# Performance work log

Hardware: AMD Instinct MI355X
Metric: run time of the kernel (lower is better)

## Reference

```python
import jax, jax.numpy as jnp
import numpy as np

N_RAYS = 8192
N_SAMPLES = 128
HIDDEN = 128
SH_DIM = 16
RAY_EXT_FACTOR = 10.0


def rsh_cart_3(d):
    # Real spherical harmonics up to degree 3, Cartesian form (16 coeffs).
    x, y, z = d[..., 0], d[..., 1], d[..., 2]
    x2, y2, z2 = x * x, y * y, z * z
    xy, yz, xz = x * y, y * z, x * z
    return jnp.stack([
        0.282094791773878 * jnp.ones_like(x),
        -0.48860251190292 * y,
        0.48860251190292 * z,
        -0.48860251190292 * x,
        1.0925484305920792 * xy,
        -1.0925484305920792 * yz,
        0.94617469575756 * z2 - 0.31539156525252,
        -1.0925484305920792 * xz,
        0.5462742152960396 * (x2 - y2),
        0.5900435899266435 * y * (-3.0 * x2 + y2),
        2.8906114426405538 * xy * z,
        0.4570457994644658 * y * (1.0 - 5.0 * z2),
        0.3731763325901154 * z * (5.0 * z2 - 3.0),
        0.4570457994644658 * x * (1.0 - 5.0 * z2),
        1.445305721320277 * z * (x2 - y2),
        0.5900435899266435 * x * (-x2 + 3.0 * y2),
    ], axis=-1)


def setup_inputs() -> dict:
    key = jax.random.key(0)
    ks = jax.random.split(key, 11)
    o = jax.random.normal(ks[0], (N_RAYS, 3), dtype=jnp.float32)
    origins = 2.5 * o / jnp.linalg.norm(o, axis=-1, keepdims=True)
    # aim roughly at the unit AABB so most rays are active
    dirs = -origins + 0.2 * jax.random.normal(ks[1], (N_RAYS, 3), dtype=jnp.float32)
    u = jax.random.uniform(ks[2], (N_RAYS, N_SAMPLES), dtype=jnp.float32)
    s1 = 1.0 / np.sqrt(3.0)
    s2 = 1.0 / np.sqrt(HIDDEN)
    s3 = 1.0 / np.sqrt(HIDDEN + SH_DIM)
    return {
        'origins': origins,
        'dirs': dirs,
        'u': u,
        'W1': s1 * jax.random.normal(ks[3], (3, HIDDEN), dtype=jnp.float32),
        'b1': jnp.zeros((HIDDEN,), jnp.float32),
        'W2': s2 * jax.random.normal(ks[4], (HIDDEN, HIDDEN), dtype=jnp.float32),
        'b2': jnp.zeros((HIDDEN,), jnp.float32),
        'Wd': s2 * jax.random.normal(ks[5], (HIDDEN, 1), dtype=jnp.float32),
        'bd': jnp.zeros((1,), jnp.float32),
        'Wc': s3 * jax.random.normal(ks[6], (HIDDEN + SH_DIM, 3), dtype=jnp.float32),
        'bc': jnp.zeros((3,), jnp.float32),
    }


def reference(origins, dirs, u, W1, b1, W2, b2, Wd, bd, Wc, bc):
    B, T = u.shape
    # ---- AABB ([-1,1]^3) slab intersection -> tnear/tfar, active mask ----
    inv_d = 1.0 / dirs
    t1 = (-1.0 - origins) * inv_d
    t2 = (1.0 - origins) * inv_d
    tnear = jnp.maximum(jnp.max(jnp.minimum(t1, t2), axis=-1), 0.0)  # (B,)
    tfar = jnp.min(jnp.maximum(t1, t2), axis=-1)                      # (B,)
    active = tfar > tnear                                             # (B,)
    tfar_c = jnp.maximum(tfar, tnear + 1e-3)
    # ---- stratified ray step sampling ----
    frac = (jnp.arange(T, dtype=u.dtype) + u) / T                     # (B,T)
    ts = tnear[:, None] + (tfar_c - tnear)[:, None] * frac            # (B,T)
    xyz = origins[:, None, :] + dirs[:, None, :] * ts[..., None]      # (B,T,3)
    # aabb is [-1,1]^3 so ndc == xyz; spatial filter = bounds test
    xyz_ndc = xyz
    mask = jnp.all(jnp.abs(xyz_ndc) <= 1.0, axis=-1) & active[:, None]  # (B,T)
    dnorm = jnp.linalg.norm(dirs, axis=-1)                            # (B,)
    ynm = rsh_cart_3(dirs / dnorm[:, None])                           # (B,16)
    # ---- radiance field MLP over all sample points ----
    x = xyz_ndc.reshape(B * T, 3)
    h = jax.nn.relu(x @ W1 + b1)
    h = jax.nn.relu(h @ W2 + b2)
    sigma = jax.nn.softplus(h @ Wd + bd).reshape(B, T)
    cond = jnp.broadcast_to(ynm[:, None, :], (B, T, SH_DIM)).reshape(B * T, SH_DIM)
    color = jax.nn.sigmoid(jnp.concatenate([h, cond], axis=-1) @ Wc + bc).reshape(B, T, 3)
    # zero out points rejected by the spatial filter (torch writes only masked)
    sigma = sigma * mask
    color = color * mask[..., None]
    # ---- transmittance integration (integrate_timesteps) ----
    tfinal = tfar_c * RAY_EXT_FACTOR
    deltas = jnp.diff(ts, axis=-1, append=tfinal[:, None])            # (B,T)
    sd = sigma * deltas * dnorm[:, None]
    csum = jnp.cumsum(sd, axis=-1)
    # weights_i = T_i * alpha_i = exp(-csum_{i-1}) - exp(-csum_i)
    weights = jnp.exp(sd - csum) - jnp.exp(-csum)                     # (B,T)
    color_out = jnp.einsum('bt,btc->bc', weights, color)              # (B,3)
    alpha_out = jnp.sum(weights, axis=-1, keepdims=True)              # (B,1)
    rgba = jnp.concatenate([color_out, alpha_out], axis=-1)           # (B,4)
    return jnp.where(active[:, None], rgba, 0.0)
```

## Files before the change

### kernel.cpp

```cpp
#include <hip/hip_runtime.h>
#include <math.h>

#define NRAYS 8192
#define T 128
#define H 128
#define SHD 16

using short8 = __attribute__((ext_vector_type(8))) short;
using f32x4  = __attribute__((ext_vector_type(4))) float;
using f32x2  = __attribute__((ext_vector_type(2))) float;
using u32x2  = __attribute__((ext_vector_type(2))) unsigned;

__device__ __forceinline__ float fexp(float x) {
  return exp2f(x * 1.44269504088896341f);
}
__device__ __forceinline__ float softplus_f(float x) {
  return fmaxf(x, 0.f) + 0.693147180559945309f * log2f(1.f + fexp(-fabsf(x)));
}
__device__ __forceinline__ float sigmoid_f(float x) {
  return __builtin_amdgcn_rcpf(1.f + fexp(-x));
}

__device__ __forceinline__ unsigned f2bf(float f) {
  unsigned u = __float_as_uint(f);
  return (u + 0x7fffu + ((u >> 16) & 1u)) >> 16;
}

__device__ __forceinline__ unsigned pk2(f32x2 h) {
  const u32x2 u = __builtin_bit_cast(u32x2, h) + (u32x2){0x8000u, 0x8000u};
  return __builtin_amdgcn_perm(u[1], u[0], 0x07060302u);
}

__global__ void preprocess(const float* __restrict__ W2, const float* __restrict__ Wd,
                           const float* __restrict__ Wc, const float* __restrict__ bc,
                           const float* __restrict__ origins, const float* __restrict__ dirs,
                           unsigned short* __restrict__ w2t,
                           unsigned short* __restrict__ woutf,
                           float* __restrict__ rayp_all) {
  const int t = blockIdx.x * 256 + threadIdx.x;
  if (t < 16384) {
    const int n = t >> 7, p = t & 127;
    const int o = (p >> 3) ^ (n & 7);
    const int k = o * 8 + (p & 7);
    w2t[t] = (unsigned short)f2bf(W2[k * 128 + n]);
  }
  if (t < 2048) {
    const int kk = t >> 9, L = (t >> 3) & 63, j = t & 7;
    const int c = L & 15, g = L >> 4;
    const int k = kk * 32 + g * 8 + j;
    float v = 0.f;
    if (c == 0) v = Wd[k];
    else if (c < 4) v = Wc[k * 3 + (c - 1)];
    woutf[t] = (unsigned short)f2bf(v);
  }
  if (t < NRAYS) {
    const float ox = origins[t*3+0], oy = origins[t*3+1], oz = origins[t*3+2];
    const float dx = dirs[t*3+0],  dy = dirs[t*3+1],  dz = dirs[t*3+2];
    const float ix = 1.f/dx, iy = 1.f/dy, iz = 1.f/dz;
    const float t1x = (-1.f-ox)*ix, t2x = (1.f-ox)*ix;
    const float t1y = (-1.f-oy)*iy, t2y = (1.f-oy)*iy;
    const float t1z = (-1.f-oz)*iz, t2z = (1.f-oz)*iz;
    float tnear = fmaxf(fmaxf(fminf(t1x,t2x), fminf(t1y,t2y)), fminf(t1z,t2z));
    tnear = fmaxf(tnear, 0.f);
    const float tfar = fminf(fminf(fmaxf(t1x,t2x), fmaxf(t1y,t2y)), fmaxf(t1z,t2z));
    const bool  active = tfar > tnear;
    const float tfar_c = fmaxf(tfar, tnear + 1e-3f);
    const float dnorm = sqrtf(dx*dx + dy*dy + dz*dz);
    const float nx = dx/dnorm, ny = dy/dnorm, nz = dz/dnorm;
    const float x2 = nx*nx, y2 = ny*ny, z2 = nz*nz;
    const float xy = nx*ny, yz = ny*nz, xz = nx*nz;
    float ynm[16];
    ynm[0]  = 0.282094791773878f;
    ynm[1]  = -0.48860251190292f*ny;
    ynm[2]  = 0.48860251190292f*nz;
    ynm[3]  = -0.48860251190292f*nx;
    ynm[4]  = 1.0925484305920792f*xy;
    ynm[5]  = -1.0925484305920792f*yz;
    ynm[6]  = 0.94617469575756f*z2 - 0.31539156525252f;
    ynm[7]  = -1.0925484305920792f*xz;
    ynm[8]  = 0.5462742152960396f*(x2-y2);
    ynm[9]  = 0.5900435899266435f*ny*(-3.f*x2+y2);
    ynm[10] = 2.8906114426405538f*xy*nz;
    ynm[11] = 0.4570457994644658f*ny*(1.f-5.f*z2);
    ynm[12] = 0.3731763325901154f*nz*(5.f*z2-3.f);
    ynm[13] = 0.4570457994644658f*nx*(1.f-5.f*z2);
    ynm[14] = 1.445305721320277f*nz*(x2-y2);
    ynm[15] = 0.5900435899266435f*nx*(-x2+3.f*y2);
    float cp0 = bc[0], cp1 = bc[1], cp2 = bc[2];
    #pragma unroll
    for (int s = 0; s < SHD; ++s) {
      cp0 = fmaf(ynm[s], Wc[(H+s)*3+0], cp0);
      cp1 = fmaf(ynm[s], Wc[(H+s)*3+1], cp1);
      cp2 = fmaf(ynm[s], Wc[(H+s)*3+2], cp2);
    }
    rayp_all[t*8+0] = tfar_c;
    rayp_all[t*8+1] = dnorm;
    rayp_all[t*8+2] = active ? 1.f : 0.f;
    rayp_all[t*8+3] = cp0;
    rayp_all[t*8+4] = cp1;
    rayp_all[t*8+5] = cp2;
    rayp_all[t*8+6] = tnear;
    rayp_all[t*8+7] = 0.f;
  }
}

__global__ __launch_bounds__(256, 4) void nerf_render(
    const float* __restrict__ origins, const float* __restrict__ dirs,
    const float* __restrict__ u, const float* __restrict__ W1,
    const float* __restrict__ b1, const float* __restrict__ b2,
    const float* __restrict__ bd, const unsigned short* __restrict__ w2t,
    const unsigned short* __restrict__ woutf, const float* __restrict__ rayp_all,
    float* __restrict__ out)
{
  const int ray = blockIdx.x;
  const int tid = threadIdx.x;
  const int L = tid & 63;
  const int w = tid >> 6;
  const int g = L >> 4;
  const int c = L & 15;

  __shared__ __align__(16) short Bs[16384];
  __shared__ __align__(16) short As2[4 * 640];
  __shared__ __align__(16) float baseA[H];
  __shared__ __align__(16) float slopeA[H];
  __shared__ float ts_s[T];
  __shared__ float mask_s[T];
  __shared__ float wred[2][4];
  __shared__ float wtot[2];

  const float tfar_c = rayp_all[ray*8+0];
  const float dnorm  = rayp_all[ray*8+1];
  const float actf   = rayp_all[ray*8+2];
  const float cpo0   = rayp_all[ray*8+3];
  const float cpo1   = rayp_all[ray*8+4];
  const float cpo2   = rayp_all[ray*8+5];
  const float tnear  = rayp_all[ray*8+6];

  {
    const float4* src = (const float4*)w2t;
    float4* dst = (float4*)Bs;
    #pragma unroll
    for (int i = 0; i < 8; ++i) dst[tid + i * 256] = src[tid + i * 256];
  }

  if (tid < T) {
    const int tl = tid;
    const float ox = origins[ray*3+0], oy = origins[ray*3+1], oz = origins[ray*3+2];
    const float dx = dirs[ray*3+0],  dy = dirs[ray*3+1],  dz = dirs[ray*3+2];
    const bool active = actf != 0.f;
    const float ut = u[ray*T + tl];
    const float frac = ((float)tl + ut) * (1.f/(float)T);
    const float tt = tnear + (tfar_c - tnear) * frac;
    const float px = fmaf(dx, tt, ox);
    const float py = fmaf(dy, tt, oy);
    const float pz = fmaf(dz, tt, oz);
    ts_s[tl] = tt;
    const bool m = (fabsf(px) <= 1.f) && (fabsf(py) <= 1.f) && (fabsf(pz) <= 1.f) && active;
    mask_s[tl] = m ? 1.f : 0.f;
    const float w0 = W1[tl], w1v = W1[H + tl], w2v = W1[2*H + tl];
    baseA[tl]  = fmaf(ox, w0, fmaf(oy, w1v, fmaf(oz, w2v, b1[tl])));
    slopeA[tl] = fmaf(dx, w0, fmaf(dy, w1v, dz * w2v));
  }

  f32x4 acc[2][8];
  #pragma unroll
  for (int mt = 0; mt < 8; ++mt) {
    const float4 bv = *(const float4*)&b2[mt*16 + g*4];
    #pragma unroll
    for (int tm = 0; tm < 2; ++tm) {
      acc[tm][mt][0] = bv.x; acc[tm][mt][1] = bv.y;
      acc[tm][mt][2] = bv.z; acc[tm][mt][3] = bv.w;
    }
  }
  __syncthreads();

  const float t0 = ts_s[32*w + c];
  const float t1 = ts_s[32*w + 16 + c];
  const f32x2 tz0 = {t0, t0}, tz1 = {t1, t1};
  const f32x2 zero2 = {0.f, 0.f};

  #pragma unroll
  for (int ks = 0; ks < 4; ++ks) {
    const int kb = ks*32 + g*8;
    const f32x4 bq0 = *(const f32x4*)&baseA[kb];
    const f32x4 bq1 = *(const f32x4*)&baseA[kb+4];
    const f32x4 sq0 = *(const f32x4*)&slopeA[kb];
    const f32x4 sq1 = *(const f32x4*)&slopeA[kb+4];
    const f32x2 b01 = {bq0[0], bq0[1]}, b23 = {bq0[2], bq0[3]};
    const f32x2 b45 = {bq1[0], bq1[1]}, b67 = {bq1[2], bq1[3]};
    const f32x2 s01 = {sq0[0], sq0[1]}, s23 = {sq0[2], sq0[3]};
    const f32x2 s45 = {sq1[0], sq1[1]}, s67 = {sq1[2], sq1[3]};
    const f32x2 a01 = __builtin_elementwise_max(__builtin_elementwise_fma(tz0, s01, b01), zero2);
    const f32x2 a23 = __builtin_elementwise_max(__builtin_elementwise_fma(tz0, s23, b23), zero2);
    const f32x2 a45 = __builtin_elementwise_max(__builtin_elementwise_fma(tz0, s45, b45), zero2);
    const f32x2 a67 = __builtin_elementwise_max(__builtin_elementwise_fma(tz0, s67, b67), zero2);
    const f32x2 e01 = __builtin_elementwise_max(__builtin_elementwise_fma(tz1, s01, b01), zero2);
    const f32x2 e23 = __builtin_elementwise_max(__builtin_elementwise_fma(tz1, s23, b23), zero2);
    const f32x2 e45 = __builtin_elementwise_max(__builtin_elementwise_fma(tz1, s45, b45), zero2);
    const f32x2 e67 = __builtin_elementwise_max(__builtin_elementwise_fma(tz1, s67, b67), zero2);
    union U { uint4 u; short8 s; } A0, A1;
    A0.u = make_uint4(pk2(a01), pk2(a23), pk2(a45), pk2(a67));
    A1.u = make_uint4(pk2(e01), pk2(e23), pk2(e45), pk2(e67));
    const int swb = ((ks*4 + g) ^ (c & 7)) * 8;
    #pragma unroll
    for (int mt = 0; mt < 8; ++mt) {
      const short8 wf = *(const short8*)&Bs[(mt*16 + c)*128 + swb];
      acc[0][mt] = __builtin_amdgcn_mfma_f32_16x16x32_bf16(wf, A0.s, acc[0][mt], 0, 0, 0);
      acc[1][mt] = __builtin_amdgcn_mfma_f32_16x16x32_bf16(wf, A1.s, acc[1][mt], 0, 0, 0);
    }
  }
  __syncthreads();
  float4* SredP = (float4*)Bs;

  short* As2w = As2 + w * 640;
  short8 wa[4];
  #pragma unroll
  for (int kk = 0; kk < 4; ++kk)
    wa[kk] = *(const short8*)&woutf[(kk*64 + L)*8];

  #pragma unroll
  for (int tm = 0; tm < 2; ++tm) {
    f32x4 oacc;
    oacc[0] = 0.f; oacc[1] = 0.f; oacc[2] = 0.f; oacc[3] = 0.f;
    #pragma unroll
    for (int kk = 0; kk < 4; ++kk) {
      #pragma unroll
      for (int i = 0; i < 2; ++i) {
        const f32x4 a = acc[tm][kk*2 + i];
        const f32x2 h01 = __builtin_elementwise_max((f32x2){a[0], a[1]}, zero2);
        const f32x2 h23 = __builtin_elementwise_max((f32x2){a[2], a[3]}, zero2);
        *(uint2*)&As2w[c*40 + i*16 + g*4] = make_uint2(pk2(h01), pk2(h23));
      }
      const short8 hbf = *(const short8*)&As2w[c*40 + g*8];
      oacc = __builtin_amdgcn_mfma_f32_16x16x32_bf16(wa[kk], hbf, oacc, 0, 0, 0);
    }
    if (g == 0)
      SredP[32*w + 16*tm + c] = make_float4(oacc[0], oacc[1], oacc[2], oacc[3]);
  }
  __syncthreads();

  float sd = 0.f, cc0 = 0.f, cc1 = 0.f, cc2 = 0.f;
  if (tid < T) {
    const float4 sv = SredP[tid];
    const float mk = mask_s[tid];
    const float sigma = softplus_f(sv.x + bd[0]) * mk;
    cc0 = mk * sigmoid_f(sv.y + cpo0);
    cc1 = mk * sigmoid_f(sv.z + cpo1);
    cc2 = mk * sigmoid_f(sv.w + cpo2);
    const float tt = ts_s[tid];
    const float tnext = (tid < T-1) ? ts_s[tid + 1] : tfar_c * 10.f;
    sd = sigma * (tnext - tt) * dnorm;
  }

  float val = sd;
  #pragma unroll
  for (int off = 1; off < 64; off <<= 1) {
    const float tmp = __shfl_up(val, off);
    if (L >= off) val += tmp;
  }
  if (tid < T && L == 63) wtot[w] = val;
  __syncthreads();
  const float csum = val + ((w == 1) ? wtot[0] : 0.f);

  float wgt = 0.f, wcx = 0.f, wcy = 0.f, wcz = 0.f;
  if (tid < T) {
    wgt = fexp(sd - csum) - fexp(-csum);
    wcx = wgt * cc0; wcy = wgt * cc1; wcz = wgt * cc2;
  }
  #pragma unroll
  for (int mm = 32; mm >= 1; mm >>= 1) {
    wgt += __shfl_xor(wgt, mm);
    wcx += __shfl_xor(wcx, mm);
    wcy += __shfl_xor(wcy, mm);
    wcz += __shfl_xor(wcz, mm);
  }
  if (tid < T && L == 0) {
    wred[w][0] = wgt; wred[w][1] = wcx; wred[w][2] = wcy; wred[w][3] = wcz;
  }
  __syncthreads();
  if (tid == 0) {
    const float aw = wred[0][0] + wred[1][0];
    const float o0 = wred[0][1] + wred[1][1];
    const float o1 = wred[0][2] + wred[1][2];
    const float o2 = wred[0][3] + wred[1][3];
    const bool act = actf != 0.f;
    out[ray*4+0] = act ? o0 : 0.f;
    out[ray*4+1] = act ? o1 : 0.f;
    out[ray*4+2] = act ? o2 : 0.f;
    out[ray*4+3] = act ? aw : 0.f;
  }
}

extern "C" void kernel_launch(void* const* d_in, const int* in_sizes, int n_in,
                              void* d_out, int out_size, void* d_ws, size_t ws_size,
                              hipStream_t stream) {
  const float* origins = (const float*)d_in[0];
  const float* dirs    = (const float*)d_in[1];
  const float* u       = (const float*)d_in[2];
  const float* W1      = (const float*)d_in[3];
  const float* b1      = (const float*)d_in[4];
  const float* W2      = (const float*)d_in[5];
  const float* b2      = (const float*)d_in[6];
  const float* Wd      = (const float*)d_in[7];
  const float* bd      = (const float*)d_in[8];
  const float* Wc      = (const float*)d_in[9];
  const float* bc      = (const float*)d_in[10];

  unsigned short* w2t      = (unsigned short*)d_ws;
  unsigned short* woutf    = (unsigned short*)((char*)d_ws + 32768);
  float*          rayp_all = (float*)((char*)d_ws + 36864);

  preprocess<<<64, 256, 0, stream>>>(W2, Wd, Wc, bc, origins, dirs,
                                     w2t, woutf, rayp_all);
  nerf_render<<<NRAYS, 256, 0, stream>>>(origins, dirs, u, W1, b1, b2, bd,
                                         w2t, woutf, rayp_all, (float*)d_out);
}
```

Measured before the change: 132.1 us.

## Retile hidden GEMM as 2x2 wave grid and use DPP wave scans

The 128x128 hidden-layer MFMA is re-partitioned so each wave covers 64 output neurons by 64 samples (4x4 tiles) rather than all 128 neurons by 32 samples. This halves the LDS weight-fragment loads per MFMA, and each wave now builds only four activation fragments per k-step instead of two per eight weight loads. Because the output head is split across neuron halves, partial density and color sums are written to two LDS slots and added before the activations. The shuffle-based prefix scan and reductions are replaced with DPP row/bcast scans plus readlane, which cuts cross-lane latency at the cost of more bespoke lane-control code.

```diff
diff --git a/kernel.cpp b/kernel.cpp
--- a/kernel.cpp
+++ b/kernel.cpp
@@ -29,6 +29,25 @@
 __device__ __forceinline__ unsigned pk2(f32x2 h) {
   const u32x2 u = __builtin_bit_cast(u32x2, h) + (u32x2){0x8000u, 0x8000u};
   return __builtin_amdgcn_perm(u[1], u[0], 0x07060302u);
+}
+
+template<int CTRL, int RM>
+__device__ __forceinline__ float dppadd(float v) {
+  const int t = __builtin_amdgcn_update_dpp(0, __builtin_bit_cast(int, v), CTRL, RM, 0xf, false);
+  return v + __builtin_bit_cast(float, t);
+}
+__device__ __forceinline__ float wave_iscan(float v) {
+  v = dppadd<0x111, 0xf>(v);
+  v = dppadd<0x112, 0xf>(v);
+  v = dppadd<0x114, 0xf>(v);
+  v = dppadd<0x118, 0xf>(v);
+  v = dppadd<0x142, 0xa>(v);
+  v = dppadd<0x143, 0xc>(v);
+  return v;
+}
+__device__ __forceinline__ float wave_total(float v) {
+  v = wave_iscan(v);
+  return __builtin_bit_cast(float, __builtin_amdgcn_readlane(__builtin_bit_cast(int, v), 63));
 }
 
 __global__ void preprocess(const float* __restrict__ W2, const float* __restrict__ Wd,
@@ -116,6 +135,8 @@
   const int tid = threadIdx.x;
   const int L = tid & 63;
   const int w = tid >> 6;
+  const int wh = w >> 1;
+  const int ws = w & 1;
   const int g = L >> 4;
   const int c = L & 15;
 
@@ -162,21 +183,22 @@
     slopeA[tl] = fmaf(dx, w0, fmaf(dy, w1v, dz * w2v));
   }
 
-  f32x4 acc[2][8];
-  #pragma unroll
-  for (int mt = 0; mt < 8; ++mt) {
-    const float4 bv = *(const float4*)&b2[mt*16 + g*4];
-    #pragma unroll
-    for (int tm = 0; tm < 2; ++tm) {
-      acc[tm][mt][0] = bv.x; acc[tm][mt][1] = bv.y;
-      acc[tm][mt][2] = bv.z; acc[tm][mt][3] = bv.w;
+  f32x4 acc[4][4];
+  #pragma unroll
+  for (int mi = 0; mi < 4; ++mi) {
+    const float4 bv = *(const float4*)&b2[(wh*4 + mi)*16 + g*4];
+    #pragma unroll
+    for (int tn = 0; tn < 4; ++tn) {
+      acc[tn][mi][0] = bv.x; acc[tn][mi][1] = bv.y;
+      acc[tn][mi][2] = bv.z; acc[tn][mi][3] = bv.w;
     }
   }
   __syncthreads();
 
-  const float t0 = ts_s[32*w + c];
-  const float t1 = ts_s[32*w + 16 + c];
-  const f32x2 tz0 = {t0, t0}, tz1 = {t1, t1};
+  float t_tn[4];
+  #pragma unroll
+  for (int tn = 0; tn < 4; ++tn) t_tn[tn] = ts_s[64*ws + 16*tn + c];
+
   const f32x2 zero2 = {0.f, 0.f};
 
   #pragma unroll
@@ -190,74 +212,73 @@
     const f32x2 b45 = {bq1[0], bq1[1]}, b67 = {bq1[2], bq1[3]};
     const f32x2 s01 = {sq0[0], sq0[1]}, s23 = {sq0[2], sq0[3]};
     const f32x2 s45 = {sq1[0], sq1[1]}, s67 = {sq1[2], sq1[3]};
-    const f32x2 a01 = __builtin_elementwise_max(__builtin_elementwise_fma(tz0, s01, b01), zero2);
-    const f32x2 a23 = __builtin_elementwise_max(__builtin_elementwise_fma(tz0, s23, b23), zero2);
-    const f32x2 a45 = __builtin_elementwise_max(__builtin_elementwise_fma(tz0, s45, b45), zero2);
-    const f32x2 a67 = __builtin_elementwise_max(__builtin_elementwise_fma(tz0, s67, b67), zero2);
-    const f32x2 e01 = __builtin_elementwise_max(__builtin_elementwise_fma(tz1, s01, b01), zero2);
-    const f32x2 e23 = __builtin_elementwise_max(__builtin_elementwise_fma(tz1, s23, b23), zero2);
-    const f32x2 e45 = __builtin_elementwise_max(__builtin_elementwise_fma(tz1, s45, b45), zero2);
-    const f32x2 e67 = __builtin_elementwise_max(__builtin_elementwise_fma(tz1, s67, b67), zero2);
-    union U { uint4 u; short8 s; } A0, A1;
-    A0.u = make_uint4(pk2(a01), pk2(a23), pk2(a45), pk2(a67));
-    A1.u = make_uint4(pk2(e01), pk2(e23), pk2(e45), pk2(e67));
+
     const int swb = ((ks*4 + g) ^ (c & 7)) * 8;
-    #pragma unroll
-    for (int mt = 0; mt < 8; ++mt) {
-      const short8 wf = *(const short8*)&Bs[(mt*16 + c)*128 + swb];
-      acc[0][mt] = __builtin_amdgcn_mfma_f32_16x16x32_bf16(wf, A0.s, acc[0][mt], 0, 0, 0);
-      acc[1][mt] = __builtin_amdgcn_mfma_f32_16x16x32_bf16(wf, A1.s, acc[1][mt], 0, 0, 0);
+    short8 wf[4];
+    #pragma unroll
+    for (int mi = 0; mi < 4; ++mi)
+      wf[mi] = *(const short8*)&Bs[((wh*4 + mi)*16 + c)*128 + swb];
+
+    #pragma unroll
+    for (int tn = 0; tn < 4; ++tn) {
+      const f32x2 t2 = {t_tn[tn], t_tn[tn]};
+      const f32x2 a01 = __builtin_elementwise_max(__builtin_elementwise_fma(t2, s01, b01), zero2);
+      const f32x2 a23 = __builtin_elementwise_max(__builtin_elementwise_fma(t2, s23, b23), zero2);
+      const f32x2 a45 = __builtin_elementwise_max(__builtin_elementwise_fma(t2, s45, b45), zero2);
+      const f32x2 a67 = __builtin_elementwise_max(__builtin_elementwise_fma(t2, s67, b67), zero2);
+      union U { uint4 u; short8 s; } Bf;
+      Bf.u = make_uint4(pk2(a01), pk2(a23), pk2(a45), pk2(a67));
+      #pragma unroll
+      for (int mi = 0; mi < 4; ++mi)
+        acc[tn][mi] = __builtin_amdgcn_mfma_f32_16x16x32_bf16(wf[mi], Bf.s, acc[tn][mi], 0, 0, 0);
     }
   }
   __syncthreads();
-  float4* SredP = (float4*)Bs;
+  float4* SredH = (float4*)Bs;
 
   short* As2w = As2 + w * 640;
-  short8 wa[4];
-  #pragma unroll
-  for (int kk = 0; kk < 4; ++kk)
-    wa[kk] = *(const short8*)&woutf[(kk*64 + L)*8];
-
-  #pragma unroll
-  for (int tm = 0; tm < 2; ++tm) {
+  short8 wa2[2];
+  #pragma unroll
+  for (int i = 0; i < 2; ++i)
+    wa2[i] = *(const short8*)&woutf[((2*wh + i)*64 + L)*8];
+
+  #pragma unroll
+  for (int tn = 0; tn < 4; ++tn) {
     f32x4 oacc;
     oacc[0] = 0.f; oacc[1] = 0.f; oacc[2] = 0.f; oacc[3] = 0.f;
     #pragma unroll
-    for (int kk = 0; kk < 4; ++kk) {
+    for (int i = 0; i < 2; ++i) {
       #pragma unroll
-      for (int i = 0; i < 2; ++i) {
-        const f32x4 a = acc[tm][kk*2 + i];
+      for (int q = 0; q < 2; ++q) {
+        const int mi = 2*i + q;
+        const f32x4 a = acc[tn][mi];
         const f32x2 h01 = __builtin_elementwise_max((f32x2){a[0], a[1]}, zero2);
         const f32x2 h23 = __builtin_elementwise_max((f32x2){a[2], a[3]}, zero2);
-        *(uint2*)&As2w[c*40 + i*16 + g*4] = make_uint2(pk2(h01), pk2(h23));
+        *(uint2*)&As2w[c*40 + q*16 + g*4] = make_uint2(pk2(h01), pk2(h23));
       }
       const short8 hbf = *(const short8*)&As2w[c*40 + g*8];
-      oacc = __builtin_amdgcn_mfma_f32_16x16x32_bf16(wa[kk], hbf, oacc, 0, 0, 0);
+      oacc = __builtin_amdgcn_mfma_f32_16x16x32_bf16(wa2[i], hbf, oacc, 0, 0, 0);
     }
     if (g == 0)
-      SredP[32*w + 16*tm + c] = make_float4(oacc[0], oacc[1], oacc[2], oacc[3]);
+      SredH[wh*128 + 64*ws + 16*tn + c] = make_float4(oacc[0], oacc[1], oacc[2], oacc[3]);
   }
   __syncthreads();
 
   float sd = 0.f, cc0 = 0.f, cc1 = 0.f, cc2 = 0.f;
   if (tid < T) {
-    const float4 sv = SredP[tid];
+    const float4 sv0 = SredH[tid];
+    const float4 sv1 = SredH[128 + tid];
     const float mk = mask_s[tid];
-    const float sigma = softplus_f(sv.x + bd[0]) * mk;
-    cc0 = mk * sigmoid_f(sv.y + cpo0);
-    cc1 = mk * sigmoid_f(sv.z + cpo1);
-    cc2 = mk * sigmoid_f(sv.w + cpo2);
+    const float sigma = softplus_f(sv0.x + sv1.x + bd[0]) * mk;
+    cc0 = mk * sigmoid_f(sv0.y + sv1.y + cpo0);
+    cc1 = mk * sigmoid_f(sv0.z + sv1.z + cpo1);
+    cc2 = mk * sigmoid_f(sv0.w + sv1.w + cpo2);
     const float tt = ts_s[tid];
     const float tnext = (tid < T-1) ? ts_s[tid + 1] : tfar_c * 10.f;
     sd = sigma * (tnext - tt) * dnorm;
   }
 
-  float val = sd;
-  #pragma unroll
-  for (int off = 1; off < 64; off <<= 1) {
-    const float tmp = __shfl_up(val, off);
-    if (L >= off) val += tmp;
-  }
+  const float val = wave_iscan(sd);
   if (tid < T && L == 63) wtot[w] = val;
   __syncthreads();
   const float csum = val + ((w == 1) ? wtot[0] : 0.f);
@@ -267,15 +288,12 @@
     wgt = fexp(sd - csum) - fexp(-csum);
     wcx = wgt * cc0; wcy = wgt * cc1; wcz = wgt * cc2;
   }
-  #pragma unroll
-  for (int mm = 32; mm >= 1; mm >>= 1) {
-    wgt += __shfl_xor(wgt, mm);
-    wcx += __shfl_xor(wcx, mm);
-    wcy += __shfl_xor(wcy, mm);
-    wcz += __shfl_xor(wcz, mm);
-  }
+  const float swgt = wave_total(wgt);
+  const float swcx = wave_total(wcx);
+  const float swcy = wave_total(wcy);
+  const float swcz = wave_total(wcz);
   if (tid < T && L == 0) {
-    wred[w][0] = wgt; wred[w][1] = wcx; wred[w][2] = wcy; wred[w][3] = wcz;
+    wred[w][0] = swgt; wred[w][1] = swcx; wred[w][2] = swcy; wred[w][3] = swcz;
   }
   __syncthreads();
   if (tid == 0) {
```

Result: no change. 133.2 us (+0.9%).
